# Kernel tuning notes

Measured on AMD Instinct MI355X. Metric: run time of the kernel, lower is better.

The kernel has to match this reference:

```python
import jax, jax.numpy as jnp
import numpy as np

B, C, D, H, W = 1, 32, 64, 128, 128

def setup_inputs() -> dict:
    key = jax.random.key(0)
    k1, k2, k3 = jax.random.split(key, 3)
    z = jax.random.uniform(k1, (B, C, D, H, W), jnp.float32)          # gate in [0,1]
    _h = jax.random.normal(k2, (B, C, D, H, W), jnp.float32)          # candidate hidden
    h0 = jax.random.normal(k3, (B, C, 1, H, W), jnp.float32)          # initial state (dd=1)
    return {"z": z, "_h": _h, "h0": h0}

def reference(z, _h, h0):
    # GruDirection3d with (d1,d2,d3)=(-1,0,0): flip along D (dim 2),
    # then sequential GRU update h[t+1] = z_t * _h_t + (1 - z_t) * h[t],
    # then flip the result back.
    zf = jnp.flip(z, axis=2)
    hf = jnp.flip(_h, axis=2)
    # move scan axis (D) to the front: (D, B, C, H, W)
    zs = jnp.moveaxis(zf, 2, 0)
    hs = jnp.moveaxis(hf, 2, 0)
    h_init = h0[:, :, 0]  # (B, C, H, W)

    def step(h_prev, zh):
        zt, ht = zh
        h_new = zt * ht + (1.0 - zt) * h_prev
        return h_new, h_new

    _, h_seq = jax.lax.scan(step, h_init, (zs, hs))   # (D, B, C, H, W)
    out = jnp.moveaxis(h_seq, 0, 2)                    # (B, C, D, H, W)
    return jnp.flip(out, axis=2)
```

## Files before the change

kernel.cpp:

```cpp
#include <hip/hip_runtime.h>


#define GRU_C  32
#define GRU_D  64
#define GRU_HW (128 * 128)
#define CHUNK  8

__global__ __launch_bounds__(256) void gru_rev_scan_kernel(
    const float* __restrict__ z,
    const float* __restrict__ h,
    const float* __restrict__ h0,
    float* __restrict__ out)
{
    const int tid = blockIdx.x * blockDim.x + threadIdx.x;
    const int c = tid >> 14;
    const int p = tid & (GRU_HW - 1);

    const int base = c * (GRU_D * GRU_HW) + p;

    float hp = h0[c * GRU_HW + p];

    for (int d0 = GRU_D - CHUNK; d0 >= 0; d0 -= CHUNK) {
        float zb[CHUNK], hb[CHUNK], ob[CHUNK];

        #pragma unroll
        for (int k = 0; k < CHUNK; ++k) {
            const int idx = base + (d0 + k) * GRU_HW;
            zb[k] = z[idx];
            hb[k] = h[idx];
        }

        #pragma unroll
        for (int k = CHUNK - 1; k >= 0; --k) {
            hp = fmaf(zb[k], hb[k], (1.0f - zb[k]) * hp);
            ob[k] = hp;
        }

        #pragma unroll
        for (int k = 0; k < CHUNK; ++k) {
            __builtin_nontemporal_store(ob[k], &out[base + (d0 + k) * GRU_HW]);
        }
    }
}

extern "C" void kernel_launch(void* const* d_in, const int* in_sizes, int n_in,
                              void* d_out, int out_size, void* d_ws, size_t ws_size,
                              hipStream_t stream) {
    const float* z  = (const float*)d_in[0];
    const float* h  = (const float*)d_in[1];
    const float* h0 = (const float*)d_in[2];
    float* out = (float*)d_out;

    const int total_threads = GRU_C * GRU_HW;
    const int block = 256;
    const int grid = total_threads / block;

    gru_rev_scan_kernel<<<grid, block, 0, stream>>>(z, h, h0, out);
}
```

Measured before the change: 62.51 us.

## Double-buffer depth chunks to overlap loads with recurrence compute

Restructures the reverse scan loop into a ping-pong pair of register buffers. The next chunk of z and h is issued before the current chunk is computed and stored, with sched barriers keeping the loads from being reordered after the compute. Launch bounds also request 8 blocks per CU. The intent is to keep more memory requests in flight per thread and hide latency, at the cost of higher register usage.

```diff
diff --git a/kernel.cpp b/kernel.cpp
--- a/kernel.cpp
+++ b/kernel.cpp
@@ -6,7 +6,22 @@
 #define GRU_HW (128 * 128)
 #define CHUNK  8
 
-__global__ __launch_bounds__(256) void gru_rev_scan_kernel(
+#define LOAD_CHUNK(zb, hb, d0)                                   \
+    _Pragma("unroll")                                            \
+    for (int k = 0; k < CHUNK; ++k) {                            \
+        const int idx = base + ((d0) + k) * GRU_HW;              \
+        zb[k] = z[idx];                                          \
+        hb[k] = h[idx];                                          \
+    }
+
+#define COMPUTE_STORE(zb, hb, d0)                                \
+    _Pragma("unroll")                                            \
+    for (int k = CHUNK - 1; k >= 0; --k) {                       \
+        hp = fmaf(zb[k], hb[k], (1.0f - zb[k]) * hp);            \
+        __builtin_nontemporal_store(hp, &out[base + ((d0) + k) * GRU_HW]); \
+    }
+
+__global__ __launch_bounds__(256, 8) void gru_rev_scan_kernel(
     const float* __restrict__ z,
     const float* __restrict__ h,
     const float* __restrict__ h0,
@@ -20,27 +35,25 @@
 
     float hp = h0[c * GRU_HW + p];
 
-    for (int d0 = GRU_D - CHUNK; d0 >= 0; d0 -= CHUNK) {
-        float zb[CHUNK], hb[CHUNK], ob[CHUNK];
+    float zA[CHUNK], hA[CHUNK], zB[CHUNK], hB[CHUNK];
 
-        #pragma unroll
-        for (int k = 0; k < CHUNK; ++k) {
-            const int idx = base + (d0 + k) * GRU_HW;
-            zb[k] = z[idx];
-            hb[k] = h[idx];
-        }
+    LOAD_CHUNK(zA, hA, GRU_D - CHUNK)
+    __builtin_amdgcn_sched_barrier(0);
 
-        #pragma unroll
-        for (int k = CHUNK - 1; k >= 0; --k) {
-            hp = fmaf(zb[k], hb[k], (1.0f - zb[k]) * hp);
-            ob[k] = hp;
-        }
+    for (int d0 = GRU_D - CHUNK; d0 >= 24; d0 -= 2 * CHUNK) {
+        LOAD_CHUNK(zB, hB, d0 - CHUNK)
+        __builtin_amdgcn_sched_barrier(0);
+        COMPUTE_STORE(zA, hA, d0)
 
-        #pragma unroll
-        for (int k = 0; k < CHUNK; ++k) {
-            __builtin_nontemporal_store(ob[k], &out[base + (d0 + k) * GRU_HW]);
-        }
+        LOAD_CHUNK(zA, hA, d0 - 2 * CHUNK)
+        __builtin_amdgcn_sched_barrier(0);
+        COMPUTE_STORE(zB, hB, d0 - CHUNK)
     }
+
+    LOAD_CHUNK(zB, hB, 0)
+    __builtin_amdgcn_sched_barrier(0);
+    COMPUTE_STORE(zA, hA, CHUNK)
+    COMPUTE_STORE(zB, hB, 0)
 }
 
 extern "C" void kernel_launch(void* const* d_in, const int* in_sizes, int n_in,
```

After: 120.1 us. +92.0%, slower.
